# Kernel optimization log

Hardware: AMD Instinct MI355X
Metric: run time of the kernel (lower is better)

## Reference

```python
import jax, jax.numpy as jnp
import numpy as np

NUM_HEADS = 16
ROPE_BASE = 10000.0

def _rope(x):
    # x: [B, H, N, D], rotates interleaved even/odd pairs
    B, H, N, D = x.shape
    pos = jnp.arange(N, dtype=jnp.float32)
    inv_freq = 1.0 / (ROPE_BASE ** (jnp.arange(0, D, 2, dtype=jnp.float32) / D))
    freqs = pos[:, None] * inv_freq[None, :]            # [N, D/2]
    cos = jnp.cos(freqs)
    sin = jnp.sin(freqs)
    xr = x.reshape(B, H, N, D // 2, 2)
    xe, xo = xr[..., 0], xr[..., 1]
    out = jnp.stack([xe * cos - xo * sin, xe * sin + xo * cos], axis=-1)
    return out.reshape(B, H, N, D)

def setup_inputs() -> dict:
    key = jax.random.key(0)
    k1, k2, k3 = jax.random.split(key, 3)
    B, N, C = 2, 2048, 1024
    x = jax.random.normal(k1, (B, N, C), dtype=jnp.float32)
    w_qkv = jax.random.normal(k2, (3 * C, C), dtype=jnp.float32) * 0.02
    w_proj = jax.random.normal(k3, (C, C), dtype=jnp.float32) * 0.02
    b_proj = jnp.zeros((C,), dtype=jnp.float32)
    return {"x": x, "w_qkv": w_qkv, "w_proj": w_proj, "b_proj": b_proj}

def reference(x, w_qkv, w_proj, b_proj):
    B, N, C = x.shape
    H = NUM_HEADS
    hd = C // H
    scale = hd ** -0.5
    qkv = jnp.einsum('bnc,dc->bnd', x, w_qkv)           # torch Linear: x @ W.T
    qkv = qkv.reshape(B, N, 3, H, hd).transpose(2, 0, 3, 1, 4)  # [3,B,H,N,hd]
    q, k, v = qkv[0], qkv[1], qkv[2]
    # rope_dim == head_dim, so whole head is rotated
    q = _rope(q)
    k = _rope(k)
    attn = jnp.einsum('bhqd,bhkd->bhqk', q, k) * scale
    attn = jax.nn.softmax(attn, axis=-1)
    out = jnp.einsum('bhqk,bhkd->bhqd', attn, v)
    out = out.transpose(0, 2, 1, 3).reshape(B, N, C)
    return jnp.einsum('bnc,dc->bnd', out, w_proj) + b_proj
```

## Files before the change

kernel.cpp:

```cpp
#include <hip/hip_runtime.h>

typedef unsigned short u16;
typedef unsigned int u32;
typedef __attribute__((ext_vector_type(8))) short bf16x8;
typedef __attribute__((ext_vector_type(4))) float f32x4;
typedef __attribute__((ext_vector_type(16))) float f32x16;

#define LOG2E 1.4426950408889634f

__device__ __forceinline__ u16 f2b(float f) {
  union { float f; u32 u; } v; v.f = f;
  u32 r = v.u + 0x7FFFu + ((v.u >> 16) & 1u);
  return (u16)(r >> 16);
}
__device__ __forceinline__ float b2f(u16 b) {
  union { u32 u; float f; } v; v.u = ((u32)b) << 16;
  return v.f;
}
__device__ __forceinline__ u32 pk2(float lo, float hi) {
  u32 r;
  asm("v_cvt_pk_bf16_f32 %0, %1, %2" : "=v"(r) : "v"(lo), "v"(hi));
  return r;
}
__device__ __forceinline__ float ex2(float x) { return __builtin_amdgcn_exp2f(x); }
__device__ __forceinline__ float rcp(float x) { return __builtin_amdgcn_rcpf(x); }

__device__ __forceinline__ void gload16(const void* g, void* l) {
  __builtin_amdgcn_global_load_lds(
      (const __attribute__((address_space(1))) u32*)g,
      (__attribute__((address_space(3))) u32*)l, 16, 0, 0);
}

__device__ __forceinline__ f32x16 mfma32(bf16x8 a, bf16x8 b, f32x16 c) {
  return __builtin_amdgcn_mfma_f32_32x32x16_bf16(a, b, c, 0, 0, 0);
}

__global__ __launch_bounds__(256) void k_cvt3(
    const float* __restrict__ s0, u16* __restrict__ d0, int n0,
    const float* __restrict__ s1, u16* __restrict__ d1, int n1,
    const float* __restrict__ s2, u16* __restrict__ d2, int n2) {
  int i = blockIdx.x * 256 + threadIdx.x;
  const int stride = gridDim.x * 256;
  const int total = n0 + n1 + n2;
  for (; i < total; i += stride) {
    const float4* s; ushort4* d; int j = i;
    if (j < n0)              { s = (const float4*)s0; d = (ushort4*)d0; }
    else if ((j -= n0) < n1) { s = (const float4*)s1; d = (ushort4*)d1; }
    else { j -= n1;            s = (const float4*)s2; d = (ushort4*)d2; }
    float4 v = s[j];
    ushort4 o;
    o.x = f2b(v.x); o.y = f2b(v.y); o.z = f2b(v.z); o.w = f2b(v.w);
    d[j] = o;
  }
}

template<int OUTMODE, int BN>
__global__ __launch_bounds__(256, 4) void k_gemm_bt(
    const u16* __restrict__ A, const u16* __restrict__ Bw,
    void* __restrict__ Cout, const float* __restrict__ bias,
    int M, int N, int K) {
  constexpr int NT = BN / 32;
  constexpr int BCH = BN / 32;
  __shared__ __align__(16) u16 As[128 * 64];
  __shared__ __align__(16) u16 Bs[BN * 64];
  const int tid = threadIdx.x;
  const int lane = tid & 63, w = tid >> 6;
  const int wr = w >> 1, wc = w & 1;
  const int g = lane >> 4, r16 = lane & 15, l7 = lane & 7;
  const int bm = blockIdx.y, bn = blockIdx.x;
  const int co[2] = { (g ^ l7) * 8, ((4 | g) ^ l7) * 8 };

  f32x4 acc[4][NT] = {};
  const int LCl = w * 64 + lane;

  for (int k0 = 0; k0 < K; k0 += 64) {
    __syncthreads();
#pragma unroll
    for (int i = 0; i < 4; ++i) {
      int LC = i * 256 + LCl;
      int row = LC >> 3;
      int c = (LC & 7) ^ (row & 7);
      gload16(A + (bm * 128 + row) * K + k0 + c * 8, As + (i * 256 + w * 64) * 8);
    }
#pragma unroll
    for (int i = 0; i < BCH; ++i) {
      int LC = i * 256 + LCl;
      int row = LC >> 3;
      int c = (LC & 7) ^ (row & 7);
      gload16(Bw + (bn * BN + row) * K + k0 + c * 8, Bs + (i * 256 + w * 64) * 8);
    }
    __syncthreads();
#pragma unroll
    for (int s = 0; s < 2; ++s) {
      bf16x8 af[4], bfr[NT];
#pragma unroll
      for (int t = 0; t < 4; ++t)
        af[t] = *(const bf16x8*)&As[(wr * 64 + t * 16 + r16) * 64 + co[s]];
#pragma unroll
      for (int t = 0; t < NT; ++t)
        bfr[t] = *(const bf16x8*)&Bs[(wc * (BN / 2) + t * 16 + r16) * 64 + co[s]];
#pragma unroll
      for (int mt = 0; mt < 4; ++mt)
#pragma unroll
        for (int nt = 0; nt < NT; ++nt)
          acc[mt][nt] = __builtin_amdgcn_mfma_f32_16x16x32_bf16(
              af[mt], bfr[nt], acc[mt][nt], 0, 0, 0);
    }
  }

  const int mbase = bm * 128 + wr * 64 + g * 4;
  const int nbase = bn * BN + wc * (BN / 2) + r16;
  if (OUTMODE == 0) {
    u16* C = (u16*)Cout;
#pragma unroll
    for (int mt = 0; mt < 4; ++mt)
#pragma unroll
      for (int nt = 0; nt < NT; ++nt)
#pragma unroll
        for (int r = 0; r < 4; ++r)
          C[(mbase + mt * 16 + r) * N + nbase + nt * 16] = f2b(acc[mt][nt][r]);
  } else {
    float* C = (float*)Cout;
    float bv[NT];
#pragma unroll
    for (int nt = 0; nt < NT; ++nt) bv[nt] = bias[nbase + nt * 16];
#pragma unroll
    for (int mt = 0; mt < 4; ++mt)
#pragma unroll
      for (int nt = 0; nt < NT; ++nt)
#pragma unroll
        for (int r = 0; r < 4; ++r)
          C[(mbase + mt * 16 + r) * N + nbase + nt * 16] = acc[mt][nt][r] + bv[nt];
  }
}

__global__ __launch_bounds__(256) void k_reorg(const u16* __restrict__ qkv,
    u16* __restrict__ Q, u16* __restrict__ K, u16* __restrict__ Vt) {
  __shared__ u16 vsh[64 * 72];
  const int bh = blockIdx.y, nt = blockIdx.x;
  const int b = bh >> 4, h = bh & 15;
  const int tid = threadIdx.x;
  const int nl = tid >> 2, c4 = tid & 3;
  const int n = nt * 64 + nl;
  const int srow = (b * 2048 + n) * 3072 + h * 64 + c4 * 16;

  float cs[8], sn[8];
#pragma unroll
  for (int p = 0; p < 8; ++p) {
    int c = c4 * 8 + p;
    float invf = exp2f(-0.41524101186092035f * (float)c);
    float ang = (float)n * invf;
    sincosf(ang, &sn[p], &cs[p]);
  }

#pragma unroll
  for (int sel = 0; sel < 2; ++sel) {
    union { uint4 v[2]; u16 s[16]; } in, out;
    const uint4* sp = (const uint4*)(qkv + srow + sel * 1024);
    in.v[0] = sp[0]; in.v[1] = sp[1];
    const float scale = sel ? 1.0f : (0.125f * LOG2E);
#pragma unroll
    for (int p = 0; p < 8; ++p) {
      float xe = b2f(in.s[2 * p]), xo = b2f(in.s[2 * p + 1]);
      out.s[2 * p]     = f2b((xe * cs[p] - xo * sn[p]) * scale);
      out.s[2 * p + 1] = f2b((xe * sn[p] + xo * cs[p]) * scale);
    }
    u16* dp = (sel ? K : Q) + (bh * 2048 + n) * 64 + c4 * 16;
    ((uint4*)dp)[0] = out.v[0];
    ((uint4*)dp)[1] = out.v[1];
  }

  {
    const uint4* sp = (const uint4*)(qkv + srow + 2048);
    uint4 v0 = sp[0], v1 = sp[1];
    *(uint4*)&vsh[nl * 72 + c4 * 16] = v0;
    *(uint4*)&vsh[nl * 72 + c4 * 16 + 8] = v1;
  }
  __syncthreads();
  {
    const int d = tid >> 2, nc = tid & 3;
    union { uint4 v[2]; u16 s[16]; } o;
#pragma unroll
    for (int j = 0; j < 16; ++j) o.s[j] = vsh[(nc * 16 + j) * 72 + d];
    u16* dp = Vt + (bh * 64 + d) * 2048 + nt * 64 + nc * 16;
    ((uint4*)dp)[0] = o.v[0];
    ((uint4*)dp)[1] = o.v[1];
  }
}

__global__ __launch_bounds__(256, 4) void k_attn(
    const u16* __restrict__ Q, const u16* __restrict__ K,
    const u16* __restrict__ Vt, u16* __restrict__ Ao) {
  __shared__ __align__(16) u16 SH[4][64 * 64];
  const int tid = threadIdx.x;
  const int lane = tid & 63, w = tid >> 6;
  const int l31 = lane & 31, hi = lane >> 5;
  const int qpair = w >> 1, kvh = w & 1;
  const int bh = blockIdx.y, qt = blockIdx.x;
  const int rr = l31 & 7;
  const int u = hi ^ (rr & 1);
  const int v = (rr >> 1) & 3;

  const int qrow = qt * 64 + qpair * 32 + l31;
  const u16* Qb = Q + (bh * 2048 + qrow) * 64 + 8 * hi;
  bf16x8 qf[4];
#pragma unroll
  for (int ks = 0; ks < 4; ++ks) qf[ks] = *(const bf16x8*)(Qb + 16 * ks);

  float z0 = 0.f;
  asm volatile("" : "+v"(z0));
  f32x16 zv;
#pragma unroll
  for (int r = 0; r < 16; ++r) zv[r] = z0;

  const u16 *kg0, *kg1, *vg0, *vg1;
  {
    int LC = tid, row = LC >> 3, c = (LC & 7) ^ (row & 7);
    kg0 = K + (bh * 2048 + row) * 64 + c * 8;
    vg0 = Vt + (bh * 64 + row) * 2048 + c * 8;
    int LC1 = 256 + tid, row1 = LC1 >> 3, c1 = (LC1 & 7) ^ (row1 & 7);
    kg1 = K + (bh * 2048 + row1) * 64 + c1 * 8;
    vg1 = Vt + (bh * 64 + row1) * 2048 + c1 * 8;
  }

  const int krowK = (kvh * 32 + l31) * 128;
  const int vrow0 = l31 * 128, vrow1 = (32 + l31) * 128;

  f32x16 acc0 = {}, acc1 = {};
  float lrun = 0.f;

  gload16(kg0, SH[0] + tid * 8);
  gload16(kg1, SH[0] + (256 + tid) * 8);
  gload16(vg0, SH[2] + tid * 8);
  gload16(vg1, SH[2] + (256 + tid) * 8);
  kg0 += 4096; kg1 += 4096; vg0 += 64; vg1 += 64;
  asm volatile("s_waitcnt vmcnt(0)" ::: "memory");
  __builtin_amdgcn_s_barrier();

#pragma unroll 2
  for (int it = 0; it < 32; ++it) {
    const int cur = it & 1;
    if (it < 31) {
      gload16(kg0, SH[cur ^ 1] + tid * 8);
      gload16(kg1, SH[cur ^ 1] + (256 + tid) * 8);
      gload16(vg0, SH[2 + (cur ^ 1)] + tid * 8);
      gload16(vg1, SH[2 + (cur ^ 1)] + (256 + tid) * 8);
      kg0 += 4096; kg1 += 4096; vg0 += 64; vg1 += 64;
    }

    const char* Kb = (const char*)SH[cur];
    const char* Vb = (const char*)SH[2 + cur];

    f32x16 st;
    __builtin_amdgcn_s_setprio(1);
    {
      const int coff = (2 * v + u) << 4;
      bf16x8 ka = *(const bf16x8*)(Kb + krowK + coff);
      st = mfma32(ka, qf[0], zv);
    }
#pragma unroll
    for (int ks = 1; ks < 4; ++ks) {
      const int coff = (2 * (ks ^ v) + u) << 4;
      bf16x8 ka = *(const bf16x8*)(Kb + krowK + coff);
      st = mfma32(ka, qf[ks], st);
    }
    __builtin_amdgcn_s_setprio(0);

    float ls[4];
    u32 W[4][2];
#pragma unroll
    for (int s = 0; s < 4; ++s) {
      float pa = ex2(st[4 * s + 0]);
      float pb = ex2(st[4 * s + 1]);
      float pc = ex2(st[4 * s + 2]);
      float pd = ex2(st[4 * s + 3]);
      ls[s] = (pa + pb) + (pc + pd);
      W[s][0] = pk2(pa, pb);
      W[s][1] = pk2(pc, pd);
    }
    lrun += (ls[0] + ls[1]) + (ls[2] + ls[3]);

    __builtin_amdgcn_s_setprio(1);
#pragma unroll
    for (int ku = 0; ku < 2; ++ku) {
      u32 a0 = W[2 * ku][0], b0 = W[2 * ku + 1][0];
      u32 a1 = W[2 * ku][1], b1 = W[2 * ku + 1][1];
      asm volatile("v_permlane32_swap_b32 %0, %1" : "+&v"(a0), "+v"(b0));
      asm volatile("v_permlane32_swap_b32 %0, %1" : "+&v"(a1), "+v"(b1));
      union { u32 wd[4]; bf16x8 v8; } pbu;
      pbu.wd[0] = a0; pbu.wd[1] = a1; pbu.wd[2] = b0; pbu.wd[3] = b1;
      const int j = 2 * kvh + ku;
      const int coff = (2 * (j ^ v) + u) << 4;
      bf16x8 va0 = *(const bf16x8*)(Vb + vrow0 + coff);
      bf16x8 va1 = *(const bf16x8*)(Vb + vrow1 + coff);
      acc0 = mfma32(va0, pbu.v8, acc0);
      acc1 = mfma32(va1, pbu.v8, acc1);
    }
    __builtin_amdgcn_s_setprio(0);

    asm volatile("s_waitcnt vmcnt(0)" ::: "memory");
    __builtin_amdgcn_s_barrier();
  }

  float* FS = (float*)SH;
  const int sbase = (qpair * 64 + lane) * 33;
  if (kvh == 1) {
#pragma unroll
    for (int r = 0; r < 16; ++r) {
      FS[sbase + r] = acc0[r];
      FS[sbase + 16 + r] = acc1[r];
    }
    FS[8000 + qpair * 64 + lane] = lrun;
  }
  __syncthreads();
  if (kvh == 0) {
#pragma unroll
    for (int r = 0; r < 16; ++r) {
      acc0[r] += FS[sbase + r];
      acc1[r] += FS[sbase + 16 + r];
    }
    lrun += FS[8000 + qpair * 64 + lane];
    float lo = __shfl_xor(lrun, 32);
    float sc = rcp(lrun + lo);

    const int m = (bh >> 4) * 2048 + qrow;
    u16* orow = Ao + m * 1024 + (bh & 15) * 64 + 4 * hi;
#pragma unroll
    for (int s = 0; s < 4; ++s) {
      uint2 o0, o1;
      o0.x = pk2(acc0[4 * s + 0] * sc, acc0[4 * s + 1] * sc);
      o0.y = pk2(acc0[4 * s + 2] * sc, acc0[4 * s + 3] * sc);
      *(uint2*)(orow + 8 * s) = o0;
      o1.x = pk2(acc1[4 * s + 0] * sc, acc1[4 * s + 1] * sc);
      o1.y = pk2(acc1[4 * s + 2] * sc, acc1[4 * s + 3] * sc);
      *(uint2*)(orow + 32 + 8 * s) = o1;
    }
  }
}

extern "C" void kernel_launch(void* const* d_in, const int* in_sizes, int n_in,
                              void* d_out, int out_size, void* d_ws, size_t ws_size,
                              hipStream_t stream) {
  (void)in_sizes; (void)n_in; (void)out_size; (void)ws_size;
  const float* x      = (const float*)d_in[0];
  const float* w_qkv  = (const float*)d_in[1];
  const float* w_proj = (const float*)d_in[2];
  const float* b_proj = (const float*)d_in[3];
  float* out = (float*)d_out;

  char* W = (char*)d_ws;
  u16* xb     = (u16*)(W + 0);
  u16* attnb  = (u16*)(W + 0);
  u16* wqkvb  = (u16*)(W + (8u  << 20));
  u16* wprojb = (u16*)(W + (14u << 20));
  u16* qkvb   = (u16*)(W + (16u << 20));
  u16* Qws    = (u16*)(W + (40u << 20));
  u16* Kws    = (u16*)(W + (48u << 20));
  u16* Vtws   = (u16*)(W + (56u << 20));

  k_cvt3<<<2048, 256, 0, stream>>>(x, xb, (4096 * 1024) / 4,
                                   w_qkv, wqkvb, (3072 * 1024) / 4,
                                   w_proj, wprojb, (1024 * 1024) / 4);
  k_gemm_bt<0, 96><<<dim3(32, 32), 256, 0, stream>>>(
      xb, wqkvb, (void*)qkvb, nullptr, 4096, 3072, 1024);
  k_reorg<<<dim3(32, 32), 256, 0, stream>>>(qkvb, Qws, Kws, Vtws);
  k_attn<<<dim3(32, 32), 256, 0, stream>>>(Qws, Kws, Vtws, attnb);
  k_gemm_bt<1, 32><<<dim3(32, 32), 256, 0, stream>>>(
      attnb, wprojb, (void*)out, b_proj, 4096, 1024, 1024);
}
```

Measured before the change: 111.0 us.

## Triple-buffer K/V tiles in attention loop with two-deep prefetch

```diff
diff --git a/kernel.cpp b/kernel.cpp
--- a/kernel.cpp
+++ b/kernel.cpp
@@ -188,10 +188,10 @@
   }
 }
 
-__global__ __launch_bounds__(256, 4) void k_attn(
+__global__ __launch_bounds__(256, 3) void k_attn(
     const u16* __restrict__ Q, const u16* __restrict__ K,
     const u16* __restrict__ Vt, u16* __restrict__ Ao) {
-  __shared__ __align__(16) u16 SH[4][64 * 64];
+  __shared__ __align__(16) u16 SH[6][64 * 64];
   const int tid = threadIdx.x;
   const int lane = tid & 63, w = tid >> 6;
   const int l31 = lane & 31, hi = lane >> 5;
@@ -229,78 +229,86 @@
   f32x16 acc0 = {}, acc1 = {};
   float lrun = 0.f;
 
-  gload16(kg0, SH[0] + tid * 8);
-  gload16(kg1, SH[0] + (256 + tid) * 8);
-  gload16(vg0, SH[2] + tid * 8);
-  gload16(vg1, SH[2] + (256 + tid) * 8);
-  kg0 += 4096; kg1 += 4096; vg0 += 64; vg1 += 64;
-  asm volatile("s_waitcnt vmcnt(0)" ::: "memory");
+#pragma unroll
+  for (int t = 0; t < 2; ++t) {
+    gload16(kg0, SH[t] + tid * 8);
+    gload16(kg1, SH[t] + (256 + tid) * 8);
+    gload16(vg0, SH[3 + t] + tid * 8);
+    gload16(vg1, SH[3 + t] + (256 + tid) * 8);
+    kg0 += 4096; kg1 += 4096; vg0 += 64; vg1 += 64;
+  }
+  asm volatile("s_waitcnt vmcnt(4)" ::: "memory");
   __builtin_amdgcn_s_barrier();
 
-#pragma unroll 2
-  for (int it = 0; it < 32; ++it) {
-    const int cur = it & 1;
-    if (it < 31) {
-      gload16(kg0, SH[cur ^ 1] + tid * 8);
-      gload16(kg1, SH[cur ^ 1] + (256 + tid) * 8);
-      gload16(vg0, SH[2 + (cur ^ 1)] + tid * 8);
-      gload16(vg1, SH[2 + (cur ^ 1)] + (256 + tid) * 8);
-      kg0 += 4096; kg1 += 4096; vg0 += 64; vg1 += 64;
-    }
-
-    const char* Kb = (const char*)SH[cur];
-    const char* Vb = (const char*)SH[2 + cur];
-
-    f32x16 st;
-    __builtin_amdgcn_s_setprio(1);
-    {
-      const int coff = (2 * v + u) << 4;
-      bf16x8 ka = *(const bf16x8*)(Kb + krowK + coff);
-      st = mfma32(ka, qf[0], zv);
-    }
-#pragma unroll
-    for (int ks = 1; ks < 4; ++ks) {
-      const int coff = (2 * (ks ^ v) + u) << 4;
-      bf16x8 ka = *(const bf16x8*)(Kb + krowK + coff);
-      st = mfma32(ka, qf[ks], st);
-    }
-    __builtin_amdgcn_s_setprio(0);
-
-    float ls[4];
-    u32 W[4][2];
-#pragma unroll
-    for (int s = 0; s < 4; ++s) {
-      float pa = ex2(st[4 * s + 0]);
-      float pb = ex2(st[4 * s + 1]);
-      float pc = ex2(st[4 * s + 2]);
-      float pd = ex2(st[4 * s + 3]);
-      ls[s] = (pa + pb) + (pc + pd);
-      W[s][0] = pk2(pa, pb);
-      W[s][1] = pk2(pc, pd);
-    }
-    lrun += (ls[0] + ls[1]) + (ls[2] + ls[3]);
-
-    __builtin_amdgcn_s_setprio(1);
-#pragma unroll
-    for (int ku = 0; ku < 2; ++ku) {
-      u32 a0 = W[2 * ku][0], b0 = W[2 * ku + 1][0];
-      u32 a1 = W[2 * ku][1], b1 = W[2 * ku + 1][1];
-      asm volatile("v_permlane32_swap_b32 %0, %1" : "+&v"(a0), "+v"(b0));
-      asm volatile("v_permlane32_swap_b32 %0, %1" : "+&v"(a1), "+v"(b1));
-      union { u32 wd[4]; bf16x8 v8; } pbu;
-      pbu.wd[0] = a0; pbu.wd[1] = a1; pbu.wd[2] = b0; pbu.wd[3] = b1;
-      const int j = 2 * kvh + ku;
-      const int coff = (2 * (j ^ v) + u) << 4;
-      bf16x8 va0 = *(const bf16x8*)(Vb + vrow0 + coff);
-      bf16x8 va1 = *(const bf16x8*)(Vb + vrow1 + coff);
-      acc0 = mfma32(va0, pbu.v8, acc0);
-      acc1 = mfma32(va1, pbu.v8, acc1);
-    }
-    __builtin_amdgcn_s_setprio(0);
-
-    asm volatile("s_waitcnt vmcnt(0)" ::: "memory");
-    __builtin_amdgcn_s_barrier();
-  }
+#define ATTN_STEP(RB, SB, DO_STAGE, WAIT0)                                     \
+  do {                                                                         \
+    if (DO_STAGE) {                                                            \
+      gload16(kg0, SH[SB] + tid * 8);                                          \
+      gload16(kg1, SH[SB] + (256 + tid) * 8);                                  \
+      gload16(vg0, SH[3 + SB] + tid * 8);                                      \
+      gload16(vg1, SH[3 + SB] + (256 + tid) * 8);                              \
+      kg0 += 4096; kg1 += 4096; vg0 += 64; vg1 += 64;                          \
+    }                                                                          \
+    const char* Kb = (const char*)SH[RB];                                      \
+    const char* Vb = (const char*)SH[3 + RB];                                  \
+    f32x16 st;                                                                 \
+    __builtin_amdgcn_s_setprio(1);                                             \
+    {                                                                          \
+      const int coff = (2 * v + u) << 4;                                       \
+      bf16x8 ka = *(const bf16x8*)(Kb + krowK + coff);                         \
+      st = mfma32(ka, qf[0], zv);                                              \
+    }                                                                          \
+    _Pragma("unroll")                                                          \
+    for (int ks = 1; ks < 4; ++ks) {                                           \
+      const int coff = (2 * (ks ^ v) + u) << 4;                                \
+      bf16x8 ka = *(const bf16x8*)(Kb + krowK + coff);                         \
+      st = mfma32(ka, qf[ks], st);                                             \
+    }                                                                          \
+    __builtin_amdgcn_s_setprio(0);                                             \
+    float ls[4];                                                               \
+    u32 W[4][2];                                                               \
+    _Pragma("unroll")                                                          \
+    for (int s = 0; s < 4; ++s) {                                              \
+      float pa = ex2(st[4 * s + 0]);                                           \
+      float pb = ex2(st[4 * s + 1]);                                           \
+      float pc = ex2(st[4 * s + 2]);                                           \
+      float pd = ex2(st[4 * s + 3]);                                           \
+      ls[s] = (pa + pb) + (pc + pd);                                           \
+      W[s][0] = pk2(pa, pb);                                                   \
+      W[s][1] = pk2(pc, pd);                                                   \
+    }                                                                          \
+    lrun += (ls[0] + ls[1]) + (ls[2] + ls[3]);                                 \
+    __builtin_amdgcn_s_setprio(1);                                             \
+    _Pragma("unroll")                                                          \
+    for (int ku = 0; ku < 2; ++ku) {                                           \
+      u32 a0 = W[2 * ku][0], b0 = W[2 * ku + 1][0];                            \
+      u32 a1 = W[2 * ku][1], b1 = W[2 * ku + 1][1];                            \
+      asm volatile("v_permlane32_swap_b32 %0, %1" : "+&v"(a0), "+v"(b0));      \
+      asm volatile("v_permlane32_swap_b32 %0, %1" : "+&v"(a1), "+v"(b1));      \
+      union { u32 wd[4]; bf16x8 v8; } pbu;                                     \
+      pbu.wd[0] = a0; pbu.wd[1] = a1; pbu.wd[2] = b0; pbu.wd[3] = b1;          \
+      const int j = 2 * kvh + ku;                                              \
+      const int coff = (2 * (j ^ v) + u) << 4;                                 \
+      bf16x8 va0 = *(const bf16x8*)(Vb + vrow0 + coff);                        \
+      bf16x8 va1 = *(const bf16x8*)(Vb + vrow1 + coff);                        \
+      acc0 = mfma32(va0, pbu.v8, acc0);                                        \
+      acc1 = mfma32(va1, pbu.v8, acc1);                                        \
+    }                                                                          \
+    __builtin_amdgcn_s_setprio(0);                                             \
+    if (WAIT0) asm volatile("s_waitcnt vmcnt(0)" ::: "memory");                \
+    else       asm volatile("s_waitcnt vmcnt(4)" ::: "memory");                \
+    __builtin_amdgcn_s_barrier();                                              \
+  } while (0)
+
+#pragma unroll 1
+  for (int base = 0; base < 30; base += 3) {
+    ATTN_STEP(0, 2, 1, 0);
+    ATTN_STEP(1, 0, 1, 0);
+    ATTN_STEP(2, 1, 1, 0);
+  }
+  ATTN_STEP(0, 2, 0, 1);
+  ATTN_STEP(1, 0, 0, 1);
+#undef ATTN_STEP
 
   float* FS = (float*)SH;
   const int sbase = (qpair * 64 + lane) * 33;
```

Result: no change. 112.0 us (+0.9%).
